# Performance work log

Measured on AMD Instinct MI355X. Metric: run time of the kernel, lower is better.

Reference implementation:

```python
import jax, jax.numpy as jnp
import numpy as np

B, C, H, W = 8, 3, 1024, 1024
N, D, PS, NB, NH = 512, 256, 16, 8, 4


def _bin_matrix():
    # static radial-binning averaging matrix for a PS x (PS//2+1) rfft2 spectrum
    h, w = PS, PS // 2 + 1
    fy = np.fft.fftfreq(h)
    fx = np.linspace(0.0, 0.5, w)
    r = np.sqrt(fx[None, :] ** 2 + fy[:, None] ** 2)
    max_r = r.max() + 1e-6
    edges = np.linspace(0.0, max_r, NB + 1)
    idx = np.clip(np.searchsorted(edges, r.ravel(), side='right') - 1, 0, NB - 1)
    M = np.zeros((NB, h * w), np.float32)
    M[idx, np.arange(h * w)] = 1.0
    cnt = M.sum(1, keepdims=True)
    return M / np.maximum(cnt, 1.0)

_BIN_M = jnp.asarray(_bin_matrix())


def _ln(x, g, b, eps=1e-5):
    m = x.mean(-1, keepdims=True)
    v = x.var(-1, keepdims=True)
    return g * (x - m) / jnp.sqrt(v + eps) + b


def _gelu(x):
    return jax.nn.gelu(x, approximate=False)


def setup_inputs() -> dict:
    key = jax.random.key(0)
    ks = jax.random.split(key, 16)
    xav = lambda k, o, i: (jax.random.normal(k, (o, i)) / np.sqrt(i)).astype(jnp.float32)
    z = lambda n: jnp.zeros((n,), jnp.float32)
    o1 = lambda n: jnp.ones((n,), jnp.float32)
    FD = 2 * NB
    return {
        'image': jax.random.normal(ks[0], (B, C, H, W), jnp.float32),
        'point_coords': jax.random.uniform(ks[1], (B, N, 2), jnp.float32, 0.0, float(W)),
        'point_labels': jax.random.randint(ks[2], (B, N), 0, 2),
        'pe_w': xav(ks[3], D, D), 'pe_b': z(D),
        'type_emb': (0.02 * jax.random.normal(ks[4], (2, D))).astype(jnp.float32),
        'fbi': (1.0 + 0.1 * jax.random.normal(ks[5], (NB,))).astype(jnp.float32),
        'fe1_w': xav(ks[6], D // 2, FD), 'fe1_b': z(D // 2),
        'feln1_g': o1(D // 2), 'feln1_b': z(D // 2),
        'fe2_w': xav(ks[7], D, D // 2), 'fe2_b': z(D),
        'feln2_g': o1(D), 'feln2_b': z(D),
        'in_w': xav(ks[8], 3 * D, D), 'in_b': z(3 * D),
        'ao_w': xav(ks[9], D, D), 'ao_b': z(D),
        'n1_g': o1(D), 'n1_b': z(D),
        'f1_w': xav(ks[10], 2 * D, D), 'f1_b': z(2 * D),
        'f2_w': xav(ks[11], D, 2 * D), 'f2_b': z(D),
        'n2_g': o1(D), 'n2_b': z(D),
        'op_w': xav(ks[12], D, D), 'op_b': z(D),
    }


def reference(image, point_coords, point_labels, pe_w, pe_b, type_emb, fbi,
              fe1_w, fe1_b, feln1_g, feln1_b, fe2_w, fe2_b, feln2_g, feln2_b,
              in_w, in_b, ao_w, ao_b, n1_g, n1_b, f1_w, f1_b, f2_w, f2_b,
              n2_g, n2_b, op_w, op_b):
    Bv, Cv, Hv, Wv = image.shape
    Nv = point_coords.shape[1]
    # --- sinusoidal positional encoding (SAM style) + linear proj ---
    nc = point_coords / jnp.array([Wv, Hv], jnp.float32)
    dim_t = 10000.0 ** (2.0 * jnp.arange(D // 4, dtype=jnp.float32) / (D // 4))
    ax = (nc[..., 0:1] * (2.0 * np.pi)) / dim_t          # [B,N,D/4]
    ay = (nc[..., 1:2] * (2.0 * np.pi)) / dim_t
    pe = jnp.concatenate([jnp.sin(ax), jnp.cos(ax), jnp.sin(ay), jnp.cos(ay)], -1)
    spatial = pe @ pe_w.T + pe_b + type_emb[point_labels]  # [B,N,D]
    # --- batched per-point patch gather + rfft2 + radial binning ---
    gray = image.mean(1)                                   # [B,H,W]
    pc = jax.lax.stop_gradient(point_coords)               # .long() detaches in torch
    half = PS // 2
    px = jnp.clip(pc[..., 0].astype(jnp.int32), half, Wv - half - 1)
    py = jnp.clip(pc[..., 1].astype(jnp.int32), half, Hv - half - 1)
    off = jnp.arange(PS) - half
    rows = py[..., None] + off                             # [B,N,PS]
    cols = px[..., None] + off
    bidx = jnp.arange(Bv)[:, None, None, None]
    patches = gray[bidx, rows[..., :, None], cols[..., None, :]]  # [B,N,PS,PS]
    fft = jnp.fft.rfft2(patches, norm='ortho')             # [B,N,PS,PS//2+1]
    mag_bins = jnp.abs(fft).reshape(Bv, Nv, -1) @ _BIN_M.T    # [B,N,NB]
    ph_bins = jnp.angle(fft).reshape(Bv, Nv, -1) @ _BIN_M.T
    feat = jnp.concatenate([mag_bins * jax.nn.softmax(fbi), ph_bins], -1)  # [B,N,2*NB]
    # --- freq encoder MLP ---
    h1 = _gelu(_ln(feat @ fe1_w.T + fe1_b, feln1_g, feln1_b))
    freq = _ln(h1 @ fe2_w.T + fe2_b, feln2_g, feln2_b)     # [B,N,D]
    # --- cross-attention fusion (spatial = Q, freq = K/V) ---
    hd = D // NH
    q = (spatial @ in_w[:D].T + in_b[:D]).reshape(Bv, Nv, NH, hd)
    k = (freq @ in_w[D:2 * D].T + in_b[D:2 * D]).reshape(Bv, Nv, NH, hd)
    v = (freq @ in_w[2 * D:].T + in_b[2 * D:]).reshape(Bv, Nv, NH, hd)
    att = jax.nn.softmax(jnp.einsum('bqhd,bkhd->bhqk', q, k) / np.sqrt(hd), -1)
    o = jnp.einsum('bhqk,bkhd->bqhd', att, v).reshape(Bv, Nv, D)
    x = _ln(spatial + (o @ ao_w.T + ao_b), n1_g, n1_b)
    ffn = _gelu(x @ f1_w.T + f1_b) @ f2_w.T + f2_b
    x = _ln(x + ffn, n2_g, n2_b)
    return x @ op_w.T + op_b
```

## Files before the change

kernel.cpp:

```cpp
#include <hip/hip_runtime.h>
#include <math.h>


typedef __attribute__((ext_vector_type(8))) short short8;
typedef __attribute__((ext_vector_type(4))) float floatx4;
typedef unsigned short u16;
typedef unsigned long long u64;

__device__ __forceinline__ float gelu_f(float x) {
  return 0.5f * x * (1.0f + erff(x * 0.70710678118654752f));
}

__device__ __forceinline__ u16 bf16_rn(float x) {
  union { float f; unsigned u; } v; v.f = x;
  unsigned r = v.u + 0x7fffu + ((v.u >> 16) & 1u);
  return (u16)(r >> 16);
}

__device__ __forceinline__ void split_bf16(float x, u16& h, u16& l) {
  h = bf16_rn(x);
  union { unsigned u; float f; } hv; hv.u = ((unsigned)h) << 16;
  l = bf16_rn(x - hv.f);
}

__device__ __forceinline__ float join_bf16(u16 h, u16 l) {
  union { unsigned u; float f; } a, b;
  a.u = ((unsigned)h) << 16;
  b.u = ((unsigned)l) << 16;
  return a.f + b.f;
}

#define W_PE   0
#define W_FE1  65536
#define W_FE2  67584
#define W_IN   100352
#define W_AO   296960
#define W_F1   362496
#define W_F2   493568
#define W_OP   624640


template <int NA, int K>
__device__ __forceinline__ void mm16_swz(
    const u16* Ah, const u16* Al, const int S,
    const u16* __restrict__ Bh, const u16* __restrict__ Bl,
    floatx4* acc)
{
  const int t = threadIdx.x;
  const int w = t >> 6, lane = t & 63;
  const int lm = lane & 15, kg = lane >> 4;
  #pragma unroll
  for (int it = 0; it < K / 32; ++it) {
    const short8 a_h = *(const short8*)&Ah[lm * S + it * 32 + kg * 8];
    const short8 a_l = *(const short8*)&Al[lm * S + it * 32 + kg * 8];
    #pragma unroll
    for (int nj = 0; nj < NA; nj++) {
      const size_t wo = (size_t)(((w * NA + nj) * (K / 32) + it) * 512 + lane * 8);
      const short8 b_h = *(const short8*)&Bh[wo];
      const short8 b_l = *(const short8*)&Bl[wo];
      acc[nj] = __builtin_amdgcn_mfma_f32_16x16x32_bf16(a_h, b_h, acc[nj], 0, 0, 0);
      acc[nj] = __builtin_amdgcn_mfma_f32_16x16x32_bf16(a_h, b_l, acc[nj], 0, 0, 0);
      acc[nj] = __builtin_amdgcn_mfma_f32_16x16x32_bf16(a_l, b_h, acc[nj], 0, 0, 0);
    }
  }
}

template <int NA, int K, int NSETS>
__device__ __forceinline__ void mm16_ks(
    const u16* Ah, const u16* Al, const int S,
    const u16* __restrict__ Bh, const u16* __restrict__ Bl,
    floatx4* acc)
{
  const int t = threadIdx.x;
  const int w = t >> 6, lane = t & 63;
  const int ww = w & 3, set = w >> 2;
  const int lm = lane & 15, kg = lane >> 4;
  constexpr int ITERS = K / (32 * NSETS);
  #pragma unroll
  for (int itl = 0; itl < ITERS; ++itl) {
    const int it = set * ITERS + itl;
    const short8 a_h = *(const short8*)&Ah[lm * S + it * 32 + kg * 8];
    const short8 a_l = *(const short8*)&Al[lm * S + it * 32 + kg * 8];
    #pragma unroll
    for (int nj = 0; nj < NA; nj++) {
      const size_t wo = (size_t)(((ww * NA + nj) * (K / 32) + it) * 512 + lane * 8);
      const short8 b_h = *(const short8*)&Bh[wo];
      const short8 b_l = *(const short8*)&Bl[wo];
      acc[nj] = __builtin_amdgcn_mfma_f32_16x16x32_bf16(a_h, b_h, acc[nj], 0, 0, 0);
      acc[nj] = __builtin_amdgcn_mfma_f32_16x16x32_bf16(a_h, b_l, acc[nj], 0, 0, 0);
      acc[nj] = __builtin_amdgcn_mfma_f32_16x16x32_bf16(a_l, b_h, acc[nj], 0, 0, 0);
    }
  }
}

template <int NA>
__device__ __forceinline__ void reduce_sets(floatx4* acc, float* PART)
{
  const int t = threadIdx.x;
  const int w = t >> 6, lane = t & 63;
  const int ww = w & 3, set = w >> 2;
  const int lm = lane & 15, kg = lane >> 4;
  __syncthreads();
  if (set != 0) {
    #pragma unroll
    for (int nj = 0; nj < NA; nj++) {
      const int col = ww * (NA * 16) + nj * 16 + lm;
      #pragma unroll
      for (int r = 0; r < 4; r++)
        PART[((set - 1) * 16 + kg * 4 + r) * 260 + col] = acc[nj][r];
    }
  }
  __syncthreads();
  if (set == 0) {
    #pragma unroll
    for (int nj = 0; nj < NA; nj++) {
      const int col = ww * (NA * 16) + nj * 16 + lm;
      #pragma unroll
      for (int r = 0; r < 4; r++) {
        const int rr = kg * 4 + r;
        acc[nj][r] += PART[rr * 260 + col] + PART[(16 + rr) * 260 + col]
                    + PART[(32 + rr) * 260 + col];
      }
    }
  }
}

template <int NA>
__device__ __forceinline__ void reduce_sets2(floatx4* acc, float* PART)
{
  const int t = threadIdx.x;
  const int w = t >> 6, lane = t & 63;
  const int ww = w & 3, set = w >> 2;
  const int lm = lane & 15, kg = lane >> 4;
  __syncthreads();
  if (set == 1) {
    #pragma unroll
    for (int nj = 0; nj < NA; nj++) {
      const int col = ww * (NA * 16) + nj * 16 + lm;
      #pragma unroll
      for (int r = 0; r < 4; r++)
        PART[(kg * 4 + r) * 260 + col] = acc[nj][r];
    }
  }
  __syncthreads();
  if (set == 0) {
    #pragma unroll
    for (int nj = 0; nj < NA; nj++) {
      const int col = ww * (NA * 16) + nj * 16 + lm;
      #pragma unroll
      for (int r = 0; r < 4; r++)
        acc[nj][r] += PART[(kg * 4 + r) * 260 + col];
    }
  }
}

__device__ __forceinline__ void stage16(
    const u16* __restrict__ Gh, const u16* __restrict__ Gl,
    u16* Lh, u16* Ll)
{
  const int t = threadIdx.x;
  #pragma unroll
  for (int i = 0; i < 2; i++) {
    const int s = t + i * 256;
    const int row = s >> 5, c = (s & 31) * 8;
    *(short8*)&Lh[row * 264 + c] = *(const short8*)&Gh[(size_t)row * 256 + c];
    *(short8*)&Ll[row * 264 + c] = *(const short8*)&Gl[(size_t)row * 256 + c];
  }
  __syncthreads();
}

template <int N_, int NA>
__device__ __forceinline__ void ln_rows(const float (&v)[NA][4], float* red1, float* red2,
                                        float (&mean)[4], float (&rstd)[4])
{
  const int t = threadIdx.x;
  const int w = t >> 6;
  const int lane = t & 63;
  const int kg = lane >> 4;
  float s1[4] = {0.f,0.f,0.f,0.f}, s2[4] = {0.f,0.f,0.f,0.f};
  #pragma unroll
  for (int nj = 0; nj < NA; nj++)
    #pragma unroll
    for (int r = 0; r < 4; r++) { s1[r] += v[nj][r]; s2[r] += v[nj][r] * v[nj][r]; }
  #pragma unroll
  for (int r = 0; r < 4; r++) {
    #pragma unroll
    for (int off = 1; off < 16; off <<= 1) {
      s1[r] += __shfl_xor(s1[r], off);
      s2[r] += __shfl_xor(s2[r], off);
    }
  }
  __syncthreads();
  if ((lane & 15) == 0) {
    #pragma unroll
    for (int r = 0; r < 4; r++) {
      red1[w * 16 + kg * 4 + r] = s1[r];
      red2[w * 16 + kg * 4 + r] = s2[r];
    }
  }
  __syncthreads();
  #pragma unroll
  for (int r = 0; r < 4; r++) {
    const int rw = kg * 4 + r;
    const float a = red1[rw] + red1[16 + rw] + red1[32 + rw] + red1[48 + rw];
    const float b = red2[rw] + red2[16 + rw] + red2[32 + rw] + red2[48 + rw];
    mean[r] = a * (1.0f / N_);
    rstd[r] = rsqrtf(b * (1.0f / N_) - mean[r] * mean[r] + 1e-5f);
  }
}

template <int N_, int NA>
__device__ __forceinline__ void ln_rows16(const float (&v)[NA][4], float* red1, float* red2,
                                          float (&mean)[4], float (&rstd)[4])
{
  const int t = threadIdx.x;
  const int w = t >> 6;
  const int lane = t & 63;
  const int ww = w & 3, set = w >> 2;
  const int kg = lane >> 4;
  float s1[4] = {0.f,0.f,0.f,0.f}, s2[4] = {0.f,0.f,0.f,0.f};
  #pragma unroll
  for (int nj = 0; nj < NA; nj++)
    #pragma unroll
    for (int r = 0; r < 4; r++) { s1[r] += v[nj][r]; s2[r] += v[nj][r] * v[nj][r]; }
  #pragma unroll
  for (int r = 0; r < 4; r++) {
    #pragma unroll
    for (int off = 1; off < 16; off <<= 1) {
      s1[r] += __shfl_xor(s1[r], off);
      s2[r] += __shfl_xor(s2[r], off);
    }
  }
  __syncthreads();
  if (set == 0 && (lane & 15) == 0) {
    #pragma unroll
    for (int r = 0; r < 4; r++) {
      red1[ww * 16 + kg * 4 + r] = s1[r];
      red2[ww * 16 + kg * 4 + r] = s2[r];
    }
  }
  __syncthreads();
  if (set == 0) {
    #pragma unroll
    for (int r = 0; r < 4; r++) {
      const int rw = kg * 4 + r;
      const float a = red1[rw] + red1[16 + rw] + red1[32 + rw] + red1[48 + rw];
      const float b = red2[rw] + red2[16 + rw] + red2[32 + rw] + red2[48 + rw];
      mean[r] = a * (1.0f / N_);
      rstd[r] = rsqrtf(b * (1.0f / N_) - mean[r] * mean[r] + 1e-5f);
    }
  }
}

__device__ __forceinline__ void store_swz(
    u16* __restrict__ Wh, u16* __restrict__ Wl, const int segbase,
    const int rel, const int kshift, const float4 v)
{
  const int K = 1 << kshift;
  const int n = rel >> kshift;
  const int k = rel & (K - 1);
  const int off8 = ((n >> 4) * (K >> 5) + (k >> 5)) * 512
                 + (((k >> 3) & 3) * 16 + (n & 15)) * 8 + (k & 7);
  u16 h0,h1,h2,h3,l0,l1,l2,l3;
  split_bf16(v.x,h0,l0); split_bf16(v.y,h1,l1);
  split_bf16(v.z,h2,l2); split_bf16(v.w,h3,l3);
  *(u64*)&Wh[segbase + off8] = (u64)h0 | ((u64)h1<<16) | ((u64)h2<<32) | ((u64)h3<<48);
  *(u64*)&Wl[segbase + off8] = (u64)l0 | ((u64)l1<<16) | ((u64)l2<<32) | ((u64)l3<<48);
}

__global__ __launch_bounds__(64) void k0_prep(
    const float* __restrict__ image, const float* __restrict__ coords,
    const float* __restrict__ fbi,
    const float* __restrict__ pe_w, const float* __restrict__ fe1_w,
    const float* __restrict__ fe2_w, const float* __restrict__ in_w,
    const float* __restrict__ ao_w, const float* __restrict__ f1_w,
    const float* __restrict__ f2_w, const float* __restrict__ op_w,
    u16* __restrict__ Wh, u16* __restrict__ Wl,
    u16* __restrict__ PEh, u16* __restrict__ PEl,
    u16* __restrict__ FEATh, u16* __restrict__ FEATl)
{
  const int blk = blockIdx.x;
  const int lane = threadIdx.x;

  if (blk < 2696) {
    const int idx = (blk * 64 + lane) * 4;
    if (idx < W_FE1) {
      store_swz(Wh, Wl, W_PE, idx - W_PE, 8, *(const float4*)&pe_w[idx - W_PE]);
    } else if (idx < W_FE2) {
      const int rel = idx - W_FE1;
      const float4 v = *(const float4*)&fe1_w[rel];
      u16 h0,h1,h2,h3,l0,l1,l2,l3;
      split_bf16(v.x,h0,l0); split_bf16(v.y,h1,l1);
      split_bf16(v.z,h2,l2); split_bf16(v.w,h3,l3);
      *(u64*)&Wh[idx] = (u64)h0 | ((u64)h1<<16) | ((u64)h2<<32) | ((u64)h3<<48);
      *(u64*)&Wl[idx] = (u64)l0 | ((u64)l1<<16) | ((u64)l2<<32) | ((u64)l3<<48);
    } else if (idx < W_IN) {
      store_swz(Wh, Wl, W_FE2, idx - W_FE2, 7, *(const float4*)&fe2_w[idx - W_FE2]);
    } else if (idx < W_AO) {
      store_swz(Wh, Wl, W_IN, idx - W_IN, 8, *(const float4*)&in_w[idx - W_IN]);
    } else if (idx < W_F1) {
      store_swz(Wh, Wl, W_AO, idx - W_AO, 8, *(const float4*)&ao_w[idx - W_AO]);
    } else if (idx < W_F2) {
      store_swz(Wh, Wl, W_F1, idx - W_F1, 8, *(const float4*)&f1_w[idx - W_F1]);
    } else if (idx < W_OP) {
      store_swz(Wh, Wl, W_F2, idx - W_F2, 9, *(const float4*)&f2_w[idx - W_F2]);
    } else {
      store_swz(Wh, Wl, W_OP, idx - W_OP, 8, *(const float4*)&op_w[idx - W_OP]);
    }
    return;
  }

  const int id = blk - 2696;
  const int b  = id >> 9;
  const float pcx = coords[id * 2 + 0];
  const float pcy = coords[id * 2 + 1];

  {
    const float TWO_PI = 6.283185307179586f;
    const float dimt = expf((float)lane * 0.28782313662425572f);
    const float ax = (pcx * (1.0f / 1024.0f)) * TWO_PI / dimt;
    const float ay = (pcy * (1.0f / 1024.0f)) * TWO_PI / dimt;
    u16 h, l;
    split_bf16(sinf(ax), h, l); PEh[id*256+lane]     = h; PEl[id*256+lane]     = l;
    split_bf16(cosf(ax), h, l); PEh[id*256+lane+64]  = h; PEl[id*256+lane+64]  = l;
    split_bf16(sinf(ay), h, l); PEh[id*256+lane+128] = h; PEl[id*256+lane+128] = l;
    split_bf16(cosf(ay), h, l); PEh[id*256+lane+192] = h; PEl[id*256+lane+192] = l;
  }

  int px = (int)pcx; px = px < 8 ? 8 : (px > 1015 ? 1015 : px);
  int py = (int)pcy; py = py < 8 ? 8 : (py > 1015 ? 1015 : py);

  __shared__ float patch[256];
  __shared__ float ct[16], st[16];
  __shared__ float Gre[144], Gim[144];
  __shared__ float msum[8], psum[8];
  __shared__ int cnt8[8];
  {
    const float* img = image + (size_t)b * 3145728;
    #pragma unroll
    for (int i = 0; i < 4; i++) {
      const int p = i * 64 + lane;
      const int r = p >> 4, c = p & 15;
      const int off = (py - 8 + r) * 1024 + (px - 8 + c);
      const float s = img[off] + img[off + 1048576] + img[off + 2097152];
      patch[r * 16 + c] = s * (1.0f / 3.0f);
    }
  }
  if (lane < 16) {
    float c, s;
    if ((lane & 3) == 0) {
      const float cv[4] = {1.0f, 0.0f, -1.0f, 0.0f};
      const float sv[4] = {0.0f, -1.0f, 0.0f, 1.0f};
      c = cv[lane >> 2]; s = sv[lane >> 2];
    } else {
      const float a = -3.14159265358979f * (float)lane * 0.125f;
      c = cosf(a); s = sinf(a);
    }
    ct[lane] = c; st[lane] = s;
  }
  if (lane < 8) { msum[lane] = 0.0f; psum[lane] = 0.0f; cnt8[lane] = 0; }
  __syncthreads();

  for (int tt = lane; tt < 144; tt += 64) {
    const int y = tt / 9, kx = tt - y * 9;
    float re = 0.0f, im = 0.0f;
    #pragma unroll
    for (int x = 0; x < 16; x++) {
      const int w = (x * kx) & 15;
      const float pv = patch[y * 16 + x];
      re = fmaf(pv, ct[w], re);
      im = fmaf(pv, st[w], im);
    }
    Gre[tt] = re; Gim[tt] = im;
  }
  __syncthreads();

  for (int tt = lane; tt < 144; tt += 64) {
    const int ky = tt / 9, kx = tt - ky * 9;
    float re = 0.0f, im = 0.0f;
    #pragma unroll
    for (int y = 0; y < 16; y++) {
      const int w = (y * ky) & 15;
      const float gr = Gre[y * 9 + kx], gi = Gim[y * 9 + kx];
      re = fmaf(gr, ct[w], re);
      re = fmaf(-gi, st[w], re);
      im = fmaf(gr, st[w], im);
      im = fmaf(gi, ct[w], im);
    }
    if (((ky & 7) == 0) && ((kx & 7) == 0)) im = 0.0f;
    const float mag = sqrtf(re * re + im * im) * 0.0625f;
    const float ph  = atan2f(im, re);

    const float fy = (ky < 8) ? (float)ky * 0.0625f : (float)(ky - 16) * 0.0625f;
    const float fx = (float)kx * 0.0625f;
    const float r = sqrtf(fx * fx + fy * fy);
    const float max_r = 0.7071077811865476f;
    const float stepf = max_r * 0.125f;
    int idx = 0;
    #pragma unroll
    for (int kq = 1; kq <= 8; kq++) {
      const float e = (kq == 8) ? max_r : stepf * (float)kq;
      if (r >= e) idx = kq;
    }
    if (idx > 7) idx = 7;
    atomicAdd(&msum[idx], mag);
    atomicAdd(&psum[idx], ph);
    atomicAdd(&cnt8[idx], 1);
  }
  __syncthreads();

  if (lane < 8) {
    float fm = fbi[0];
    #pragma unroll
    for (int j = 1; j < 8; j++) fm = fmaxf(fm, fbi[j]);
    float se = 0.0f;
    #pragma unroll
    for (int j = 0; j < 8; j++) se += expf(fbi[j] - fm);
    const float smx = expf(fbi[lane] - fm) / se;
    const float c = (float)(cnt8[lane] > 0 ? cnt8[lane] : 1);
    u16 h, l;
    split_bf16((msum[lane] / c) * smx, h, l);
    FEATh[id*16+lane] = h; FEATl[id*16+lane] = l;
    split_bf16(psum[lane] / c, h, l);
    FEATh[id*16+8+lane] = h; FEATl[id*16+8+lane] = l;
  }
}

__global__ __launch_bounds__(256) void k1_front(
    const u16* __restrict__ Wh, const u16* __restrict__ Wl,
    const u16* __restrict__ PEh, const u16* __restrict__ PEl,
    const u16* __restrict__ FEATh, const u16* __restrict__ FEATl,
    const float* __restrict__ pe_b, const int* __restrict__ labels,
    const float* __restrict__ temb,
    const float* __restrict__ fe1_b, const float* __restrict__ feln1_g, const float* __restrict__ feln1_b,
    const float* __restrict__ fe2_b, const float* __restrict__ feln2_g, const float* __restrict__ feln2_b,
    u16* __restrict__ SPh, u16* __restrict__ SPl,
    u16* __restrict__ FQh, u16* __restrict__ FQl)
{
  __shared__ __align__(16) u16 smem[8448];
  __shared__ float redbuf[128];
  const int blk = blockIdx.x;
  const int t = threadIdx.x;
  const int w = t >> 6, lane = t & 63;
  const int lm = lane & 15, kg = lane >> 4;

  if (blk < 256) {
    const int m0 = blk * 16;
    u16* Lh = smem;
    u16* Ll = smem + 4224;
    stage16(PEh + (size_t)m0 * 256, PEl + (size_t)m0 * 256, Lh, Ll);
    floatx4 acc[4];
    #pragma unroll
    for (int j = 0; j < 4; j++) acc[j] = (floatx4){0.f,0.f,0.f,0.f};
    mm16_swz<4, 256>(Lh, Ll, 264, Wh + W_PE, Wl + W_PE, acc);
    #pragma unroll
    for (int nj = 0; nj < 4; nj++) {
      const int col = w * 64 + nj * 16 + lm;
      #pragma unroll
      for (int r = 0; r < 4; r++) {
        const int row = m0 + kg * 4 + r;
        const float v = acc[nj][r] + pe_b[col] + temb[labels[row] * 256 + col];
        u16 h, l; split_bf16(v, h, l);
        SPh[(size_t)row * 256 + col] = h;
        SPl[(size_t)row * 256 + col] = l;
      }
    }
    return;
  }

  const int m0 = (blk - 256) * 16;
  u16* h1h = smem;
  u16* h1l = smem + 2176;

  floatx4 acc1[2];
  acc1[0] = (floatx4){0.f,0.f,0.f,0.f};
  acc1[1] = (floatx4){0.f,0.f,0.f,0.f};
  {
    const short8 zz = {0,0,0,0,0,0,0,0};
    const short8 a_h = (kg < 2) ? *(const short8*)&FEATh[(size_t)(m0 + lm) * 16 + kg * 8] : zz;
    const short8 a_l = (kg < 2) ? *(const short8*)&FEATl[(size_t)(m0 + lm) * 16 + kg * 8] : zz;
    #pragma unroll
    for (int nj = 0; nj < 2; nj++) {
      const int col = w * 32 + nj * 16 + lm;
      const short8 b_h = (kg < 2) ? *(const short8*)&Wh[W_FE1 + (size_t)col * 16 + kg * 8] : zz;
      const short8 b_l = (kg < 2) ? *(const short8*)&Wl[W_FE1 + (size_t)col * 16 + kg * 8] : zz;
      acc1[nj] = __builtin_amdgcn_mfma_f32_16x16x32_bf16(a_h, b_h, acc1[nj], 0, 0, 0);
      acc1[nj] = __builtin_amdgcn_mfma_f32_16x16x32_bf16(a_h, b_l, acc1[nj], 0, 0, 0);
      acc1[nj] = __builtin_amdgcn_mfma_f32_16x16x32_bf16(a_l, b_h, acc1[nj], 0, 0, 0);
    }
  }

  float v1[2][4];
  #pragma unroll
  for (int nj = 0; nj < 2; nj++) {
    const int col = w * 32 + nj * 16 + lm;
    #pragma unroll
    for (int r = 0; r < 4; r++) v1[nj][r] = acc1[nj][r] + fe1_b[col];
  }
  float mean[4], rstd[4];
  ln_rows<128, 2>(v1, redbuf, redbuf + 64, mean, rstd);
  #pragma unroll
  for (int nj = 0; nj < 2; nj++) {
    const int col = w * 32 + nj * 16 + lm;
    #pragma unroll
    for (int r = 0; r < 4; r++) {
      float y = feln1_g[col] * (v1[nj][r] - mean[r]) * rstd[r] + feln1_b[col];
      y = gelu_f(y);
      u16 h, l; split_bf16(y, h, l);
      h1h[(kg * 4 + r) * 136 + col] = h;
      h1l[(kg * 4 + r) * 136 + col] = l;
    }
  }
  __syncthreads();

  floatx4 acc2[4];
  #pragma unroll
  for (int j = 0; j < 4; j++) acc2[j] = (floatx4){0.f,0.f,0.f,0.f};
  mm16_swz<4, 128>(h1h, h1l, 136, Wh + W_FE2, Wl + W_FE2, acc2);

  float v2[4][4];
  #pragma unroll
  for (int nj = 0; nj < 4; nj++) {
    const int col = w * 64 + nj * 16 + lm;
    #pragma unroll
    for (int r = 0; r < 4; r++) v2[nj][r] = acc2[nj][r] + fe2_b[col];
  }
  ln_rows<256, 4>(v2, redbuf, redbuf + 64, mean, rstd);
  #pragma unroll
  for (int nj = 0; nj < 4; nj++) {
    const int col = w * 64 + nj * 16 + lm;
    #pragma unroll
    for (int r = 0; r < 4; r++) {
      const int rw = m0 + kg * 4 + r;
      float y = feln2_g[col] * (v2[nj][r] - mean[r]) * rstd[r] + feln2_b[col];
      u16 h, l; split_bf16(y, h, l);
      FQh[(size_t)rw * 256 + col] = h;
      FQl[(size_t)rw * 256 + col] = l;
    }
  }
}

__global__ __launch_bounds__(512) void k2_qkv(
    const u16* __restrict__ Wh, const u16* __restrict__ Wl,
    const u16* __restrict__ SPh, const u16* __restrict__ SPl,
    const u16* __restrict__ FQh, const u16* __restrict__ FQl,
    const float* __restrict__ in_b,
    u16* __restrict__ Qh, u16* __restrict__ Ql,
    u16* __restrict__ Kh, u16* __restrict__ Kl,
    u16* __restrict__ Vth, u16* __restrict__ Vtl)
{
  __shared__ __align__(16) u16 smem[8448];
  __shared__ float PART[16 * 260];
  const int bx = blockIdx.x;
  const int seg = bx >> 8;
  const int m0 = (bx & 255) * 16;
  const int t = threadIdx.x;
  const int w = t >> 6, lane = t & 63;
  const int ww = w & 3, set = w >> 2;
  const int lm = lane & 15, kg = lane >> 4;

  const u16 *Ah, *Al; const u16 *Wsh, *Wsl; const float* bias;
  if (seg == 0)      { Ah = SPh; Al = SPl; Wsh = Wh + W_IN;          Wsl = Wl + W_IN;          bias = in_b; }
  else if (seg == 1) { Ah = FQh; Al = FQl; Wsh = Wh + W_IN + 65536;  Wsl = Wl + W_IN + 65536;  bias = in_b + 256; }
  else               { Ah = FQh; Al = FQl; Wsh = Wh + W_IN + 131072; Wsl = Wl + W_IN + 131072; bias = in_b + 512; }

  u16* Lh = smem;
  u16* Ll = smem + 4224;
  {
    const u16* Gh = Ah + (size_t)m0 * 256;
    const u16* Gl = Al + (size_t)m0 * 256;
    const int row = t >> 5, c = (t & 31) * 8;
    *(short8*)&Lh[row * 264 + c] = *(const short8*)&Gh[(size_t)row * 256 + c];
    *(short8*)&Ll[row * 264 + c] = *(const short8*)&Gl[(size_t)row * 256 + c];
    __syncthreads();
  }

  floatx4 acc[4];
  #pragma unroll
  for (int j = 0; j < 4; j++) acc[j] = (floatx4){0.f,0.f,0.f,0.f};
  mm16_ks<4, 256, 2>(Lh, Ll, 264, Wsh, Wsl, acc);
  reduce_sets2<4>(acc, PART);

  if (set != 0) return;

  if (seg < 2) {
    u16* oh = (seg == 0) ? Qh : Kh;
    u16* ol = (seg == 0) ? Ql : Kl;
    #pragma unroll
    for (int nj = 0; nj < 4; nj++) {
      const int col = ww * 64 + nj * 16 + lm;
      #pragma unroll
      for (int r = 0; r < 4; r++) {
        const int row = m0 + kg * 4 + r;
        u16 h, l; split_bf16(acc[nj][r] + bias[col], h, l);
        oh[(size_t)row * 256 + col] = h;
        ol[(size_t)row * 256 + col] = l;
      }
    }
  } else {
    #pragma unroll
    for (int nj = 0; nj < 4; nj++) {
      const int col = ww * 64 + nj * 16 + lm;
      u64 hp = 0, lp = 0;
      #pragma unroll
      for (int r = 0; r < 4; r++) {
        u16 h, l; split_bf16(acc[nj][r] + bias[col], h, l);
        hp |= ((u64)h) << (16 * r);
        lp |= ((u64)l) << (16 * r);
      }
      *(u64*)&Vth[(size_t)col * 4096 + m0 + kg * 4] = hp;
      *(u64*)&Vtl[(size_t)col * 4096 + m0 + kg * 4] = lp;
    }
  }
}

__global__ __launch_bounds__(512) void k3_attn(
    const u16* __restrict__ Qh, const u16* __restrict__ Ql,
    const u16* __restrict__ Kh, const u16* __restrict__ Kl,
    const u16* __restrict__ Vth, const u16* __restrict__ Vtl,
    u16* __restrict__ Oh, u16* __restrict__ Ol)
{
  __shared__ __align__(16) u16 smem[64512];
  __shared__ float O1[64 * 68];
  __shared__ float Mbuf[64], Lbuf[64];

  const int t = threadIdx.x;
  const int w = t >> 6, lane = t & 63;
  const int ww = w & 3, set = w >> 2;
  const int lm = lane & 15, kg = lane >> 4;
  const int ts = t & 255;

  u16* sQh = smem;
  u16* sQl = smem + 4608;
  u16* sKh = smem + 9216 + set * 27648;
  u16* sKl = sKh + 4608;
  u16* sVh = sKh + 9216;
  u16* sVl = sKh + 13824;
  u16* sPh = sKh + 18432;
  u16* sPl = sKh + 23040;

  const int qt = blockIdx.x & 7;
  const int bh = blockIdx.x >> 3;
  const int b = bh >> 2, h = bh & 3;
  const int qrow0 = b * 512 + qt * 64;

  {
    const int r = t >> 3, d = (t & 7) * 8;
    *(short8*)&sQh[r * 72 + d] = *(const short8*)&Qh[(size_t)(qrow0 + r) * 256 + h * 64 + d];
    *(short8*)&sQl[r * 72 + d] = *(const short8*)&Ql[(size_t)(qrow0 + r) * 256 + h * 64 + d];
  }

  float m_i[4], l_i[4];
  floatx4 o_acc[4];
  #pragma unroll
  for (int r = 0; r < 4; r++) { m_i[r] = -INFINITY; l_i[r] = 0.0f; }
  #pragma unroll
  for (int dj = 0; dj < 4; dj++) o_acc[dj] = (floatx4){0.f, 0.f, 0.f, 0.f};

  __syncthreads();
  short8 q_h[2], q_l[2];
  #pragma unroll
  for (int ks = 0; ks < 2; ks++) {
    const int off = (ww * 16 + lm) * 72 + ks * 32 + kg * 8;
    q_h[ks] = *(const short8*)&sQh[off];
    q_l[ks] = *(const short8*)&sQl[off];
  }

  for (int ktl = 0; ktl < 4; ktl++) {
    const int kt = set * 4 + ktl;
    __syncthreads();
    {
      const int krow0 = b * 512 + kt * 64;
      #pragma unroll
      for (int i = 0; i < 2; i++) {
        const int s = ts + i * 256;
        const int r = s >> 3, d = (s & 7) * 8;
        *(short8*)&sKh[r * 72 + d] = *(const short8*)&Kh[(size_t)(krow0 + r) * 256 + h * 64 + d];
        *(short8*)&sKl[r * 72 + d] = *(const short8*)&Kl[(size_t)(krow0 + r) * 256 + h * 64 + d];
        *(short8*)&sVh[r * 72 + d] = *(const short8*)&Vth[(size_t)(h * 64 + r) * 4096 + krow0 + d];
        *(short8*)&sVl[r * 72 + d] = *(const short8*)&Vtl[(size_t)(h * 64 + r) * 4096 + krow0 + d];
      }
    }
    __syncthreads();

    floatx4 sacc[4];
    #pragma unroll
    for (int nj = 0; nj < 4; nj++) sacc[nj] = (floatx4){0.f, 0.f, 0.f, 0.f};
    #pragma unroll
    for (int ks = 0; ks < 2; ks++) {
      #pragma unroll
      for (int nj = 0; nj < 4; nj++) {
        const int off = (nj * 16 + lm) * 72 + ks * 32 + kg * 8;
        const short8 kb_h = *(const short8*)&sKh[off];
        const short8 kb_l = *(const short8*)&sKl[off];
        sacc[nj] = __builtin_amdgcn_mfma_f32_16x16x32_bf16(q_h[ks], kb_h, sacc[nj], 0, 0, 0);
        sacc[nj] = __builtin_amdgcn_mfma_f32_16x16x32_bf16(q_h[ks], kb_l, sacc[nj], 0, 0, 0);
        sacc[nj] = __builtin_amdgcn_mfma_f32_16x16x32_bf16(q_l[ks], kb_h, sacc[nj], 0, 0, 0);
      }
    }

    float pp[4][4];
    #pragma unroll
    for (int r = 0; r < 4; r++) {
      float mx = -INFINITY;
      #pragma unroll
      for (int nj = 0; nj < 4; nj++) {
        sacc[nj][r] *= 0.125f;
        mx = fmaxf(mx, sacc[nj][r]);
      }
      #pragma unroll
      for (int off = 1; off < 16; off <<= 1) mx = fmaxf(mx, __shfl_xor(mx, off));
      const float mnew = fmaxf(m_i[r], mx);
      const float alpha = expf(m_i[r] - mnew);
      m_i[r] = mnew;
      float rs = 0.0f;
      #pragma unroll
      for (int nj = 0; nj < 4; nj++) { pp[nj][r] = expf(sacc[nj][r] - mnew); rs += pp[nj][r]; }
      #pragma unroll
      for (int off = 1; off < 16; off <<= 1) rs += __shfl_xor(rs, off);
      l_i[r] = l_i[r] * alpha + rs;
      #pragma unroll
      for (int dj = 0; dj < 4; dj++) o_acc[dj][r] *= alpha;
    }

    #pragma unroll
    for (int nj = 0; nj < 4; nj++)
      #pragma unroll
      for (int r = 0; r < 4; r++) {
        u16 ph, pl; split_bf16(pp[nj][r], ph, pl);
        sPh[(ww * 16 + kg * 4 + r) * 72 + nj * 16 + lm] = ph;
        sPl[(ww * 16 + kg * 4 + r) * 72 + nj * 16 + lm] = pl;
      }

    #pragma unroll
    for (int ks = 0; ks < 2; ks++) {
      const short8 p_h = *(const short8*)&sPh[(ww * 16 + lm) * 72 + ks * 32 + kg * 8];
      const short8 p_l = *(const short8*)&sPl[(ww * 16 + lm) * 72 + ks * 32 + kg * 8];
      #pragma unroll
      for (int dj = 0; dj < 4; dj++) {
        const int off = (dj * 16 + lm) * 72 + ks * 32 + kg * 8;
        const short8 v_h = *(const short8*)&sVh[off];
        const short8 v_l = *(const short8*)&sVl[off];
        o_acc[dj] = __builtin_amdgcn_mfma_f32_16x16x32_bf16(p_h, v_h, o_acc[dj], 0, 0, 0);
        o_acc[dj] = __builtin_amdgcn_mfma_f32_16x16x32_bf16(p_l, v_h, o_acc[dj], 0, 0, 0);
        o_acc[dj] = __builtin_amdgcn_mfma_f32_16x16x32_bf16(p_h, v_l, o_acc[dj], 0, 0, 0);
      }
    }
  }

  if (set == 1) {
    #pragma unroll
    for (int r = 0; r < 4; r++) {
      const int row = ww * 16 + kg * 4 + r;
      if (lm == 0) { Mbuf[row] = m_i[r]; Lbuf[row] = l_i[r]; }
      #pragma unroll
      for (int dj = 0; dj < 4; dj++)
        O1[row * 68 + dj * 16 + lm] = o_acc[dj][r];
    }
  }
  __syncthreads();
  if (set == 0) {
    #pragma unroll
    for (int r = 0; r < 4; r++) {
      const int row = ww * 16 + kg * 4 + r;
      const float m1 = Mbuf[row], l1v = Lbuf[row];
      const float mnew = fmaxf(m_i[r], m1);
      const float a0 = expf(m_i[r] - mnew);
      const float a1 = expf(m1 - mnew);
      const float inv_l = 1.0f / (l_i[r] * a0 + l1v * a1);
      const size_t rowoff = (size_t)(qrow0 + row) * 256 + h * 64;
      #pragma unroll
      for (int dj = 0; dj < 4; dj++) {
        const float val = (o_acc[dj][r] * a0 + O1[row * 68 + dj * 16 + lm] * a1) * inv_l;
        u16 hh, ll; split_bf16(val, hh, ll);
        Oh[rowoff + dj * 16 + lm] = hh;
        Ol[rowoff + dj * 16 + lm] = ll;
      }
    }
  }
}

__global__ __launch_bounds__(1024) void k4_tail(
    const u16* __restrict__ Wh, const u16* __restrict__ Wl,
    const u16* __restrict__ Oh, const u16* __restrict__ Ol,
    const u16* __restrict__ SPh, const u16* __restrict__ SPl,
    const float* __restrict__ ao_b, const float* __restrict__ n1_g, const float* __restrict__ n1_b,
    const float* __restrict__ f1_b, const float* __restrict__ f2_b,
    const float* __restrict__ n2_g, const float* __restrict__ n2_b,
    const float* __restrict__ op_b, float* __restrict__ OUT)
{
  __shared__ __align__(16) u16 smem[25088];
  __shared__ float redbuf[128];
  __shared__ float PART[3 * 16 * 260];
  u16* B1h = smem;
  u16* B1l = smem + 4224;
  u16* Fh  = smem + 8448;
  u16* Fl  = smem + 16768;

  const int t = threadIdx.x;
  const int w = t >> 6, lane = t & 63;
  const int ww = w & 3, set = w >> 2;
  const int lm = lane & 15, kg = lane >> 4;
  const int m0 = blockIdx.x * 16;

  {
    const u16* Gh = Oh + (size_t)m0 * 256;
    const u16* Gl = Ol + (size_t)m0 * 256;
    if (t < 512) {
      const int row = t >> 5, c = (t & 31) * 8;
      *(short8*)&B1h[row * 264 + c] = *(const short8*)&Gh[(size_t)row * 256 + c];
      *(short8*)&B1l[row * 264 + c] = *(const short8*)&Gl[(size_t)row * 256 + c];
    }
    __syncthreads();
  }

  floatx4 acc[4];
  #pragma unroll
  for (int j = 0; j < 4; j++) acc[j] = (floatx4){0.f,0.f,0.f,0.f};
  mm16_ks<4, 256, 4>(B1h, B1l, 264, Wh + W_AO, Wl + W_AO, acc);
  reduce_sets<4>(acc, PART);

  float x1reg[4][4];
  {
    float v[4][4];
    if (set == 0) {
      #pragma unroll
      for (int nj = 0; nj < 4; nj++) {
        const int col = ww * 64 + nj * 16 + lm;
        #pragma unroll
        for (int r = 0; r < 4; r++) {
          const size_t si = (size_t)(m0 + kg * 4 + r) * 256 + col;
          v[nj][r] = acc[nj][r] + ao_b[col] + join_bf16(SPh[si], SPl[si]);
        }
      }
    } else {
      #pragma unroll
      for (int nj = 0; nj < 4; nj++)
        #pragma unroll
        for (int r = 0; r < 4; r++) v[nj][r] = 0.0f;
    }
    float mean[4], rstd[4];
    ln_rows16<256, 4>(v, redbuf, redbuf + 64, mean, rstd);
    if (set == 0) {
      #pragma unroll
      for (int nj = 0; nj < 4; nj++) {
        const int col = ww * 64 + nj * 16 + lm;
        #pragma unroll
        for (int r = 0; r < 4; r++) {
          const float y = n1_g[col] * (v[nj][r] - mean[r]) * rstd[r] + n1_b[col];
          x1reg[nj][r] = y;
          u16 h, l; split_bf16(y, h, l);
          B1h[(kg * 4 + r) * 264 + col] = h;
          B1l[(kg * 4 + r) * 264 + col] = l;
        }
      }
    }
  }
  __syncthreads();

  #pragma unroll
  for (int ct = 0; ct < 2; ct++) {
    floatx4 a4[4];
    #pragma unroll
    for (int j = 0; j < 4; j++) a4[j] = (floatx4){0.f,0.f,0.f,0.f};
    mm16_ks<4, 256, 4>(B1h, B1l, 264,
                       Wh + W_F1 + (size_t)ct * 65536, Wl + W_F1 + (size_t)ct * 65536, a4);
    reduce_sets<4>(a4, PART);
    if (set == 0) {
      #pragma unroll
      for (int nj = 0; nj < 4; nj++) {
        const int col = ct * 256 + ww * 64 + nj * 16 + lm;
        #pragma unroll
        for (int r = 0; r < 4; r++) {
          const float y = gelu_f(a4[nj][r] + f1_b[col]);
          u16 h, l; split_bf16(y, h, l);
          Fh[(kg * 4 + r) * 520 + col] = h;
          Fl[(kg * 4 + r) * 520 + col] = l;
        }
      }
    }
  }
  __syncthreads();

  #pragma unroll
  for (int j = 0; j < 4; j++) acc[j] = (floatx4){0.f,0.f,0.f,0.f};
  mm16_ks<4, 512, 4>(Fh, Fl, 520, Wh + W_F2, Wl + W_F2, acc);
  reduce_sets<4>(acc, PART);
  {
    float v[4][4];
    if (set == 0) {
      #pragma unroll
      for (int nj = 0; nj < 4; nj++) {
        const int col = ww * 64 + nj * 16 + lm;
        #pragma unroll
        for (int r = 0; r < 4; r++)
          v[nj][r] = acc[nj][r] + f2_b[col] + x1reg[nj][r];
      }
    } else {
      #pragma unroll
      for (int nj = 0; nj < 4; nj++)
        #pragma unroll
        for (int r = 0; r < 4; r++) v[nj][r] = 0.0f;
    }
    float mean[4], rstd[4];
    ln_rows16<256, 4>(v, redbuf, redbuf + 64, mean, rstd);
    if (set == 0) {
      #pragma unroll
      for (int nj = 0; nj < 4; nj++) {
        const int col = ww * 64 + nj * 16 + lm;
        #pragma unroll
        for (int r = 0; r < 4; r++) {
          const float y = n2_g[col] * (v[nj][r] - mean[r]) * rstd[r] + n2_b[col];
          u16 h, l; split_bf16(y, h, l);
          B1h[(kg * 4 + r) * 264 + col] = h;
          B1l[(kg * 4 + r) * 264 + col] = l;
        }
      }
    }
  }
  __syncthreads();

  #pragma unroll
  for (int j = 0; j < 4; j++) acc[j] = (floatx4){0.f,0.f,0.f,0.f};
  mm16_ks<4, 256, 4>(B1h, B1l, 264, Wh + W_OP, Wl + W_OP, acc);
  reduce_sets<4>(acc, PART);
  if (set == 0) {
    #pragma unroll
    for (int nj = 0; nj < 4; nj++) {
      const int col = ww * 64 + nj * 16 + lm;
      #pragma unroll
      for (int r = 0; r < 4; r++)
        OUT[(size_t)(m0 + kg * 4 + r) * 256 + col] = acc[nj][r] + op_b[col];
    }
  }
}

extern "C" void kernel_launch(void* const* d_in, const int* in_sizes, int n_in,
                              void* d_out, int out_size, void* d_ws, size_t ws_size,
                              hipStream_t stream) {
  const float* image   = (const float*)d_in[0];
  const float* coords  = (const float*)d_in[1];
  const int*   labels  = (const int*)d_in[2];
  const float* pe_w    = (const float*)d_in[3];
  const float* pe_b    = (const float*)d_in[4];
  const float* temb    = (const float*)d_in[5];
  const float* fbi     = (const float*)d_in[6];
  const float* fe1_w   = (const float*)d_in[7];
  const float* fe1_b   = (const float*)d_in[8];
  const float* feln1_g = (const float*)d_in[9];
  const float* feln1_b = (const float*)d_in[10];
  const float* fe2_w   = (const float*)d_in[11];
  const float* fe2_b   = (const float*)d_in[12];
  const float* feln2_g = (const float*)d_in[13];
  const float* feln2_b = (const float*)d_in[14];
  const float* in_w    = (const float*)d_in[15];
  const float* in_b    = (const float*)d_in[16];
  const float* ao_w    = (const float*)d_in[17];
  const float* ao_b    = (const float*)d_in[18];
  const float* n1_g    = (const float*)d_in[19];
  const float* n1_b    = (const float*)d_in[20];
  const float* f1_w    = (const float*)d_in[21];
  const float* f1_b    = (const float*)d_in[22];
  const float* f2_w    = (const float*)d_in[23];
  const float* f2_b    = (const float*)d_in[24];
  const float* n2_g    = (const float*)d_in[25];
  const float* n2_b    = (const float*)d_in[26];
  const float* op_w    = (const float*)d_in[27];
  const float* op_b    = (const float*)d_in[28];

  float* ws = (float*)d_ws;
  u16* S = (u16*)(ws + 2 * (1u << 20));
  u16* Wh = S;
  u16* Wl = S + 690176;
  u16* PEh   = S + 1380352;  u16* PEl   = PEh + 1048576;
  u16* FEATh = S + 3477504;  u16* FEATl = FEATh + 65536;
  u16* FQh   = S + 4657152;  u16* FQl   = FQh + 1048576;
  u16* SPh   = S + 6754304;  u16* SPl   = SPh + 1048576;
  u16* Qh    = S + 8851456;  u16* Ql    = Qh + 1048576;
  u16* Kh    = S + 10948608; u16* Kl    = Kh + 1048576;
  u16* Vth   = S + 13045760; u16* Vtl   = Vth + 1048576;
  u16* Oh    = S + 15142912; u16* Ol    = Oh + 1048576;

  float* OUT = (float*)d_out;

  k0_prep<<<6792, 64, 0, stream>>>(
      image, coords, fbi, pe_w, fe1_w, fe2_w, in_w, ao_w, f1_w, f2_w, op_w,
      Wh, Wl, PEh, PEl, FEATh, FEATl);
  k1_front<<<512, 256, 0, stream>>>(
      Wh, Wl, PEh, PEl, FEATh, FEATl, pe_b, labels, temb,
      fe1_b, feln1_g, feln1_b, fe2_b, feln2_g, feln2_b,
      SPh, SPl, FQh, FQl);
  k2_qkv<<<768, 512, 0, stream>>>(
      Wh, Wl, SPh, SPl, FQh, FQl, in_b, Qh, Ql, Kh, Kl, Vth, Vtl);
  k3_attn<<<256, 512, 0, stream>>>(Qh, Ql, Kh, Kl, Vth, Vtl, Oh, Ol);
  k4_tail<<<256, 1024, 0, stream>>>(
      Wh, Wl, Oh, Ol, SPh, SPl, ao_b, n1_g, n1_b, f1_b, f2_b, n2_g, n2_b, op_b, OUT);
}
```

Baseline: 287.4 us.

## Fuse QKV projection into front kernel, eliminating k2_qkv launch and FQ buffer

The Q projection is folded into the spatial branch of k1_front, and the K and V projections into its frequency branch. Each branch now stages its freshly computed 16-row bf16 hi/lo tile in shared memory instead of writing FQ to global and re-reading it. This removes one kernel launch and the global round trip of the intermediate activations. In exchange, k1 blocks do 2-3x more GEMM work serially with 256 threads and no split-K, and use more shared memory, which may lower occupancy compared with the 768-block k2 launch.

```diff
diff --git a/kernel.cpp b/kernel.cpp
--- a/kernel.cpp
+++ b/kernel.cpp
@@ -121,35 +121,6 @@
         acc[nj][r] += PART[rr * 260 + col] + PART[(16 + rr) * 260 + col]
                     + PART[(32 + rr) * 260 + col];
       }
-    }
-  }
-}
-
-template <int NA>
-__device__ __forceinline__ void reduce_sets2(floatx4* acc, float* PART)
-{
-  const int t = threadIdx.x;
-  const int w = t >> 6, lane = t & 63;
-  const int ww = w & 3, set = w >> 2;
-  const int lm = lane & 15, kg = lane >> 4;
-  __syncthreads();
-  if (set == 1) {
-    #pragma unroll
-    for (int nj = 0; nj < NA; nj++) {
-      const int col = ww * (NA * 16) + nj * 16 + lm;
-      #pragma unroll
-      for (int r = 0; r < 4; r++)
-        PART[(kg * 4 + r) * 260 + col] = acc[nj][r];
-    }
-  }
-  __syncthreads();
-  if (set == 0) {
-    #pragma unroll
-    for (int nj = 0; nj < NA; nj++) {
-      const int col = ww * (NA * 16) + nj * 16 + lm;
-      #pragma unroll
-      for (int r = 0; r < 4; r++)
-        acc[nj][r] += PART[(kg * 4 + r) * 260 + col];
     }
   }
 }
@@ -434,10 +405,13 @@
     const float* __restrict__ temb,
     const float* __restrict__ fe1_b, const float* __restrict__ feln1_g, const float* __restrict__ feln1_b,
     const float* __restrict__ fe2_b, const float* __restrict__ feln2_g, const float* __restrict__ feln2_b,
+    const float* __restrict__ in_b,
     u16* __restrict__ SPh, u16* __restrict__ SPl,
-    u16* __restrict__ FQh, u16* __restrict__ FQl)
-{
-  __shared__ __align__(16) u16 smem[8448];
+    u16* __restrict__ Qh, u16* __restrict__ Ql,
+    u16* __restrict__ Kh, u16* __restrict__ Kl,
+    u16* __restrict__ Vth, u16* __restrict__ Vtl)
+{
+  __shared__ __align__(16) u16 smem[12800];
   __shared__ float redbuf[128];
   const int blk = blockIdx.x;
   const int t = threadIdx.x;
@@ -453,6 +427,7 @@
     #pragma unroll
     for (int j = 0; j < 4; j++) acc[j] = (floatx4){0.f,0.f,0.f,0.f};
     mm16_swz<4, 256>(Lh, Ll, 264, Wh + W_PE, Wl + W_PE, acc);
+    __syncthreads();
     #pragma unroll
     for (int nj = 0; nj < 4; nj++) {
       const int col = w * 64 + nj * 16 + lm;
@@ -463,6 +438,25 @@
         u16 h, l; split_bf16(v, h, l);
         SPh[(size_t)row * 256 + col] = h;
         SPl[(size_t)row * 256 + col] = l;
+        Lh[(kg * 4 + r) * 264 + col] = h;
+        Ll[(kg * 4 + r) * 264 + col] = l;
+      }
+    }
+    __syncthreads();
+
+    floatx4 accq[4];
+    #pragma unroll
+    for (int j = 0; j < 4; j++) accq[j] = (floatx4){0.f,0.f,0.f,0.f};
+    mm16_swz<4, 256>(Lh, Ll, 264, Wh + W_IN, Wl + W_IN, accq);
+    #pragma unroll
+    for (int nj = 0; nj < 4; nj++) {
+      const int col = w * 64 + nj * 16 + lm;
+      #pragma unroll
+      for (int r = 0; r < 4; r++) {
+        const int row = m0 + kg * 4 + r;
+        u16 h, l; split_bf16(accq[nj][r] + in_b[col], h, l);
+        Qh[(size_t)row * 256 + col] = h;
+        Ql[(size_t)row * 256 + col] = l;
       }
     }
     return;
@@ -471,6 +465,8 @@
   const int m0 = (blk - 256) * 16;
   u16* h1h = smem;
   u16* h1l = smem + 2176;
+  u16* Ah  = smem + 4352;
+  u16* Al  = smem + 8576;
 
   floatx4 acc1[2];
   acc1[0] = (floatx4){0.f,0.f,0.f,0.f};
@@ -531,80 +527,44 @@
     const int col = w * 64 + nj * 16 + lm;
     #pragma unroll
     for (int r = 0; r < 4; r++) {
-      const int rw = m0 + kg * 4 + r;
       float y = feln2_g[col] * (v2[nj][r] - mean[r]) * rstd[r] + feln2_b[col];
       u16 h, l; split_bf16(y, h, l);
-      FQh[(size_t)rw * 256 + col] = h;
-      FQl[(size_t)rw * 256 + col] = l;
-    }
-  }
-}
-
-__global__ __launch_bounds__(512) void k2_qkv(
-    const u16* __restrict__ Wh, const u16* __restrict__ Wl,
-    const u16* __restrict__ SPh, const u16* __restrict__ SPl,
-    const u16* __restrict__ FQh, const u16* __restrict__ FQl,
-    const float* __restrict__ in_b,
-    u16* __restrict__ Qh, u16* __restrict__ Ql,
-    u16* __restrict__ Kh, u16* __restrict__ Kl,
-    u16* __restrict__ Vth, u16* __restrict__ Vtl)
-{
-  __shared__ __align__(16) u16 smem[8448];
-  __shared__ float PART[16 * 260];
-  const int bx = blockIdx.x;
-  const int seg = bx >> 8;
-  const int m0 = (bx & 255) * 16;
-  const int t = threadIdx.x;
-  const int w = t >> 6, lane = t & 63;
-  const int ww = w & 3, set = w >> 2;
-  const int lm = lane & 15, kg = lane >> 4;
-
-  const u16 *Ah, *Al; const u16 *Wsh, *Wsl; const float* bias;
-  if (seg == 0)      { Ah = SPh; Al = SPl; Wsh = Wh + W_IN;          Wsl = Wl + W_IN;          bias = in_b; }
-  else if (seg == 1) { Ah = FQh; Al = FQl; Wsh = Wh + W_IN + 65536;  Wsl = Wl + W_IN + 65536;  bias = in_b + 256; }
-  else               { Ah = FQh; Al = FQl; Wsh = Wh + W_IN + 131072; Wsl = Wl + W_IN + 131072; bias = in_b + 512; }
-
-  u16* Lh = smem;
-  u16* Ll = smem + 4224;
+      Ah[(kg * 4 + r) * 264 + col] = h;
+      Al[(kg * 4 + r) * 264 + col] = l;
+    }
+  }
+  __syncthreads();
+
   {
-    const u16* Gh = Ah + (size_t)m0 * 256;
-    const u16* Gl = Al + (size_t)m0 * 256;
-    const int row = t >> 5, c = (t & 31) * 8;
-    *(short8*)&Lh[row * 264 + c] = *(const short8*)&Gh[(size_t)row * 256 + c];
-    *(short8*)&Ll[row * 264 + c] = *(const short8*)&Gl[(size_t)row * 256 + c];
-    __syncthreads();
-  }
-
-  floatx4 acc[4];
-  #pragma unroll
-  for (int j = 0; j < 4; j++) acc[j] = (floatx4){0.f,0.f,0.f,0.f};
-  mm16_ks<4, 256, 2>(Lh, Ll, 264, Wsh, Wsl, acc);
-  reduce_sets2<4>(acc, PART);
-
-  if (set != 0) return;
-
-  if (seg < 2) {
-    u16* oh = (seg == 0) ? Qh : Kh;
-    u16* ol = (seg == 0) ? Ql : Kl;
+    floatx4 acck[4];
+    #pragma unroll
+    for (int j = 0; j < 4; j++) acck[j] = (floatx4){0.f,0.f,0.f,0.f};
+    mm16_swz<4, 256>(Ah, Al, 264, Wh + W_IN + 65536, Wl + W_IN + 65536, acck);
     #pragma unroll
     for (int nj = 0; nj < 4; nj++) {
-      const int col = ww * 64 + nj * 16 + lm;
+      const int col = w * 64 + nj * 16 + lm;
       #pragma unroll
       for (int r = 0; r < 4; r++) {
         const int row = m0 + kg * 4 + r;
-        u16 h, l; split_bf16(acc[nj][r] + bias[col], h, l);
-        oh[(size_t)row * 256 + col] = h;
-        ol[(size_t)row * 256 + col] = l;
-      }
-    }
-  } else {
+        u16 h, l; split_bf16(acck[nj][r] + in_b[256 + col], h, l);
+        Kh[(size_t)row * 256 + col] = h;
+        Kl[(size_t)row * 256 + col] = l;
+      }
+    }
+  }
+
+  {
+    floatx4 accv[4];
+    #pragma unroll
+    for (int j = 0; j < 4; j++) accv[j] = (floatx4){0.f,0.f,0.f,0.f};
+    mm16_swz<4, 256>(Ah, Al, 264, Wh + W_IN + 131072, Wl + W_IN + 131072, accv);
     #pragma unroll
     for (int nj = 0; nj < 4; nj++) {
-      const int col = ww * 64 + nj * 16 + lm;
+      const int col = w * 64 + nj * 16 + lm;
       u64 hp = 0, lp = 0;
       #pragma unroll
       for (int r = 0; r < 4; r++) {
-        u16 h, l; split_bf16(acc[nj][r] + bias[col], h, l);
+        u16 h, l; split_bf16(accv[nj][r] + in_b[512 + col], h, l);
         hp |= ((u64)h) << (16 * r);
         lp |= ((u64)l) << (16 * r);
       }
@@ -974,7 +934,6 @@
   u16* Wl = S + 690176;
   u16* PEh   = S + 1380352;  u16* PEl   = PEh + 1048576;
   u16* FEATh = S + 3477504;  u16* FEATl = FEATh + 65536;
-  u16* FQh   = S + 4657152;  u16* FQl   = FQh + 1048576;
   u16* SPh   = S + 6754304;  u16* SPl   = SPh + 1048576;
   u16* Qh    = S + 8851456;  u16* Ql    = Qh + 1048576;
   u16* Kh    = S + 10948608; u16* Kl    = Kh + 1048576;
@@ -988,10 +947,8 @@
       Wh, Wl, PEh, PEl, FEATh, FEATl);
   k1_front<<<512, 256, 0, stream>>>(
       Wh, Wl, PEh, PEl, FEATh, FEATl, pe_b, labels, temb,
-      fe1_b, feln1_g, feln1_b, fe2_b, feln2_g, feln2_b,
-      SPh, SPl, FQh, FQl);
-  k2_qkv<<<768, 512, 0, stream>>>(
-      Wh, Wl, SPh, SPl, FQh, FQl, in_b, Qh, Ql, Kh, Kl, Vth, Vtl);
+      fe1_b, feln1_g, feln1_b, fe2_b, feln2_g, feln2_b, in_b,
+      SPh, SPl, Qh, Ql, Kh, Kl, Vth, Vtl);
   k3_attn<<<256, 512, 0, stream>>>(Qh, Ql, Kh, Kl, Vth, Vtl, Oh, Ol);
   k4_tail<<<256, 1024, 0, stream>>>(
       Wh, Wl, Oh, Ol, SPh, SPl, ao_b, n1_g, n1_b, f1_b, f2_b, n2_g, n2_b, op_b, OUT);
```

Measured after the change: 289.0 us. About the same (+0.5%).
